# Kernel tuning notes

Measured on AMD Instinct MI355X. Metric: run time of the kernel, lower is better.

Reference implementation:

```python
import jax, jax.numpy as jnp
import numpy as np

N = 4096
BATCH = 256
N_IO = 16
EPS = 1.1920929e-07  # torch RMSNorm default eps = finfo(float32).eps


def setup_inputs() -> dict:
    key = jax.random.key(0)
    k_x, k_w = jax.random.split(key)
    x_input = jax.random.normal(k_x, (BATCH, N), dtype=jnp.float32)
    # orthogonal init for W
    a = jax.random.normal(k_w, (N, N), dtype=jnp.float32)
    q, r = jnp.linalg.qr(a)
    W = q * jnp.sign(jnp.diag(r))[None, :]
    B = jnp.zeros((N,), dtype=jnp.float32)
    input_scale = jnp.ones((N_IO,), dtype=jnp.float32)
    output_scale = jnp.ones((N_IO,), dtype=jnp.float32)
    norm_weight = jnp.ones((N,), dtype=jnp.float32)  # RMSNorm elementwise affine
    input_pos = jnp.arange(N_IO, dtype=jnp.int32)            # ids 0..15
    output_pos = jnp.arange(N_IO, dtype=jnp.int32) + (N - N_IO)  # ids 4080..4095
    return {
        "x_input": x_input, "W": W, "B": B,
        "input_scale": input_scale, "output_scale": output_scale,
        "norm_weight": norm_weight,
        "input_pos": input_pos, "output_pos": output_pos,
        "steps": 16,
    }


def reference(x_input, W, B, input_scale, output_scale, norm_weight,
              input_pos, output_pos, steps):
    # dropout is identity in eval mode (rate 0.0)
    def step(h, inj):
        signal = h @ W + B + inj                      # [batch, N]
        a = jnp.tanh(signal)
        ms = jnp.mean(a * a, axis=-1, keepdims=True)
        return a * jax.lax.rsqrt(ms + EPS) * norm_weight

    # pulse mode: scaled input injected only at t == 0
    inj0 = x_input.at[:, input_pos].multiply(input_scale)
    h0 = jnp.zeros_like(x_input)                      # fresh state
    h1 = step(h0, inj0)

    def body(h, _):
        hn = step(h, 0.0)
        return hn, hn

    h_final, rest = jax.lax.scan(body, h1, None, length=steps - 1)  # rest: [steps-1, batch, N]
    outs = jnp.concatenate([h1[:, None, :], jnp.swapaxes(rest, 0, 1)], axis=1)  # [batch, steps, N]
    outs = outs.at[:, :, output_pos].multiply(output_scale)
    return outs, h_final
```

## Files before the change

kernel.cpp:

```cpp
#include <hip/hip_runtime.h>
#include <hip/hip_bf16.h>

#define BATCH 256
#define NDIM  4096
#define STEPS 16
#define EPS_RMS 1.1920929e-07f

typedef _Float16 f16x8 __attribute__((ext_vector_type(8)));
typedef float  f32x4  __attribute__((ext_vector_type(4)));
typedef unsigned short u16x4 __attribute__((ext_vector_type(4)));
typedef unsigned int   u32x4 __attribute__((ext_vector_type(4)));

#define AS1 __attribute__((address_space(1)))
#define AS3 __attribute__((address_space(3)))
#define GLDS16(gp, lp) __builtin_amdgcn_global_load_lds( \
    (const AS1 void*)(gp), (AS3 void*)(lp), 16, 0, 0)
#define SBAR() do { asm volatile("" ::: "memory"); \
                    __builtin_amdgcn_s_barrier();  \
                    asm volatile("" ::: "memory"); } while (0)

__device__ __forceinline__ unsigned short f2h(float f) {
  _Float16 h = (_Float16)f;
  union { _Float16 h; unsigned short u; } v; v.h = h; return v.u;
}

__device__ __forceinline__ float block_reduce_sum_512(float v) {
  __shared__ float ws[8];
  __shared__ float tot;
  #pragma unroll
  for (int off = 32; off > 0; off >>= 1) v += __shfl_down(v, off, 64);
  int lane = threadIdx.x & 63, w = threadIdx.x >> 6;
  if (lane == 0) ws[w] = v;
  __syncthreads();
  if (threadIdx.x == 0) {
    float t = 0.f;
    #pragma unroll
    for (int i = 0; i < 8; ++i) t += ws[i];
    tot = t;
  }
  __syncthreads();
  return tot;
}

__global__ __launch_bounds__(256) void transpose_w(
    const float* __restrict__ W, unsigned short* __restrict__ Wt) {
  __shared__ float tile[64][65];
  int n0 = blockIdx.x * 64;
  int k0 = blockIdx.y * 64;
  int t = threadIdx.x;
  int r = t >> 4, c4 = (t & 15) * 4;
  #pragma unroll
  for (int p = 0; p < 4; ++p) {
    f32x4 v = *(const f32x4*)(W + (size_t)(k0 + r + 16 * p) * NDIM + n0 + c4);
    tile[r + 16 * p][c4 + 0] = v[0];
    tile[r + 16 * p][c4 + 1] = v[1];
    tile[r + 16 * p][c4 + 2] = v[2];
    tile[r + 16 * p][c4 + 3] = v[3];
  }
  __syncthreads();
  #pragma unroll
  for (int p = 0; p < 4; ++p) {
    int nr = r + 16 * p;
    u16x4 o;
    #pragma unroll
    for (int j = 0; j < 4; ++j) o[j] = f2h(tile[c4 + j][nr]);
    *(u16x4*)(Wt + (size_t)(n0 + nr) * NDIM + k0 + c4) = o;
  }
}

__global__ void init_colmul(const float* __restrict__ iscale,
                            const float* __restrict__ oscale,
                            const int* __restrict__ ipos, const int* __restrict__ opos,
                            float* __restrict__ icm, float* __restrict__ ocm) {
  int c = blockIdx.x * 256 + threadIdx.x;
  if (c >= NDIM) return;
  float iv = 1.f, ov = 1.f;
  #pragma unroll
  for (int i = 0; i < 16; ++i) {
    if (ipos[i] == c) iv *= iscale[i];
    if (opos[i] == c) ov *= oscale[i];
  }
  icm[c] = iv; ocm[c] = ov;
}

__global__ __launch_bounds__(512) void step0_kernel(
    const float* __restrict__ x, const float* __restrict__ bias,
    const float* __restrict__ icm, const float* __restrict__ nw,
    const float* __restrict__ ocm,
    unsigned short* __restrict__ hbuf, float* __restrict__ out) {
  int row = blockIdx.x;
  int tid = threadIdx.x;
  const float* xr = x + (size_t)row * NDIM;
  float a[8];
  float sq = 0.f;
  #pragma unroll
  for (int p = 0; p < 2; ++p) {
    int c = p * 2048 + tid * 4;
    f32x4 xv = *(const f32x4*)(xr + c);
    f32x4 bv = *(const f32x4*)(bias + c);
    f32x4 ic = *(const f32x4*)(icm + c);
    #pragma unroll
    for (int j = 0; j < 4; ++j) {
      float av = tanhf(bv[j] + xv[j] * ic[j]);
      a[p * 4 + j] = av;
      sq += av * av;
    }
  }
  float tot = block_reduce_sum_512(sq);
  float scale = rsqrtf(tot * (1.0f / NDIM) + EPS_RMS);
  unsigned short* hrow = hbuf + (size_t)row * NDIM;
  float* orow = out + (size_t)row * STEPS * NDIM;
  #pragma unroll
  for (int p = 0; p < 2; ++p) {
    int c = p * 2048 + tid * 4;
    f32x4 nv = *(const f32x4*)(nw + c);
    f32x4 oc = *(const f32x4*)(ocm + c);
    u16x4 hs; f32x4 os;
    #pragma unroll
    for (int j = 0; j < 4; ++j) {
      float h = a[p * 4 + j] * scale * nv[j];
      hs[j] = f2h(h);
      os[j] = h * oc[j];
    }
    *(u16x4*)(hrow + c) = hs;
    *(f32x4*)(orow + c) = os;
  }
}

__global__ __launch_bounds__(256, 2) void gemm_kernel(
    const unsigned short* __restrict__ A,
    const unsigned short* __restrict__ Bt,
    float* __restrict__ pbuf) {
  __shared__ __align__(16) unsigned short As[2][64 * 64];
  __shared__ __align__(16) unsigned short Bs[2][128 * 64];
  const int tid = threadIdx.x;
  const int n0 = blockIdx.x * 128;
  const int m0 = blockIdx.y * 64;
  const int ks = blockIdx.z;
  const int kbase = ks * 1024;
  const int wave = tid >> 6, lane = tid & 63;
  const int wm = (wave >> 1) * 32, wn = (wave & 1) * 64;
  const int l15 = lane & 15;
  const int g = lane >> 4;
  const int q = l15 & 7;
  const int rho = lane >> 3;
  const int koff = ((lane & 7) ^ rho) * 8;

  const unsigned short* aP[2];
  const unsigned short* bP[4];
  #pragma unroll
  for (int i = 0; i < 2; ++i)
    aP[i] = A + (size_t)(m0 + wave * 16 + i * 8 + rho) * NDIM + kbase + koff;
  #pragma unroll
  for (int i = 0; i < 4; ++i)
    bP[i] = Bt + (size_t)(n0 + wave * 32 + i * 8 + rho) * NDIM + kbase + koff;

  f32x4 acc[2][4];
  f32x4 zero = {0.f, 0.f, 0.f, 0.f};
  #pragma unroll
  for (int i = 0; i < 2; ++i)
    #pragma unroll
    for (int j = 0; j < 4; ++j) acc[i][j] = zero;

  #pragma unroll
  for (int i = 0; i < 2; ++i)
    GLDS16(aP[i], &As[0][(wave * 16 + i * 8) * 64]);
  #pragma unroll
  for (int i = 0; i < 4; ++i)
    GLDS16(bP[i], &Bs[0][(wave * 32 + i * 8) * 64]);

  for (int it = 0; it < 16; ++it) {
    const int p = it & 1;
    SBAR();
    if (it < 15) {
      const int kb = (it + 1) * 64;
      #pragma unroll
      for (int i = 0; i < 2; ++i)
        GLDS16(aP[i] + kb, &As[1 - p][(wave * 16 + i * 8) * 64]);
      #pragma unroll
      for (int i = 0; i < 4; ++i)
        GLDS16(bP[i] + kb, &Bs[1 - p][(wave * 32 + i * 8) * 64]);
      asm volatile("s_waitcnt vmcnt(6)" ::: "memory");
    } else {
      asm volatile("s_waitcnt vmcnt(0)" ::: "memory");
    }
    SBAR();
    #pragma unroll
    for (int kk = 0; kk < 2; ++kk) {
      f16x8 af[2], bfr[4];
      #pragma unroll
      for (int mf = 0; mf < 2; ++mf) {
        int row = wm + mf * 16 + l15;
        af[mf] = *(const f16x8*)&As[p][row * 64 + (((kk << 2) + g) ^ q) * 8];
      }
      #pragma unroll
      for (int nf = 0; nf < 4; ++nf) {
        int row = wn + nf * 16 + l15;
        bfr[nf] = *(const f16x8*)&Bs[p][row * 64 + (((kk << 2) + g) ^ q) * 8];
      }
      #pragma unroll
      for (int mf = 0; mf < 2; ++mf)
        #pragma unroll
        for (int nf = 0; nf < 4; ++nf)
          acc[mf][nf] = __builtin_amdgcn_mfma_f32_16x16x32_f16(af[mf], bfr[nf], acc[mf][nf], 0, 0, 0);
    }
  }

  float* pout = pbuf + (size_t)ks * BATCH * NDIM;
  const int crow = (lane >> 4) * 4;
  #pragma unroll
  for (int mf = 0; mf < 2; ++mf) {
    #pragma unroll
    for (int nf = 0; nf < 4; ++nf) {
      int col = n0 + wn + nf * 16 + l15;
      #pragma unroll
      for (int r = 0; r < 4; ++r) {
        int row = m0 + wm + mf * 16 + crow + r;
        pout[(size_t)row * NDIM + col] = acc[mf][nf][r];
      }
    }
  }
}

__global__ __launch_bounds__(512) void normalize_kernel(
    const float* __restrict__ pbuf, const float* __restrict__ bias,
    const float* __restrict__ nw, const float* __restrict__ ocm,
    unsigned short* __restrict__ hbuf, float* __restrict__ out,
    float* __restrict__ hfin, int t, int is_last) {
  const size_t SL = (size_t)BATCH * NDIM;
  int row = blockIdx.x;
  int tid = threadIdx.x;
  const float* p0 = pbuf + (size_t)row * NDIM;
  float a[8];
  float sq = 0.f;
  #pragma unroll
  for (int p = 0; p < 2; ++p) {
    int c = p * 2048 + tid * 4;
    f32x4 s = *(const f32x4*)(p0 + c);
    s += *(const f32x4*)(p0 + SL + c);
    s += *(const f32x4*)(p0 + 2 * SL + c);
    s += *(const f32x4*)(p0 + 3 * SL + c);
    f32x4 bv = *(const f32x4*)(bias + c);
    #pragma unroll
    for (int j = 0; j < 4; ++j) {
      float av = tanhf(s[j] + bv[j]);
      a[p * 4 + j] = av;
      sq += av * av;
    }
  }
  float tot = block_reduce_sum_512(sq);
  float scale = rsqrtf(tot * (1.0f / NDIM) + EPS_RMS);
  unsigned short* hrow = hbuf + (size_t)row * NDIM;
  float* orow = out + ((size_t)row * STEPS + t) * NDIM;
  #pragma unroll
  for (int p = 0; p < 2; ++p) {
    int c = p * 2048 + tid * 4;
    f32x4 nv = *(const f32x4*)(nw + c);
    f32x4 oc = *(const f32x4*)(ocm + c);
    u16x4 hs; f32x4 os; f32x4 hv;
    #pragma unroll
    for (int j = 0; j < 4; ++j) {
      float h = a[p * 4 + j] * scale * nv[j];
      hv[j] = h;
      hs[j] = f2h(h);
      os[j] = h * oc[j];
    }
    *(u16x4*)(hrow + c) = hs;
    *(f32x4*)(orow + c) = os;
    if (is_last) *(f32x4*)(hfin + (size_t)row * NDIM + c) = hv;
  }
}

extern "C" void kernel_launch(void* const* d_in, const int* in_sizes, int n_in,
                              void* d_out, int out_size, void* d_ws, size_t ws_size,
                              hipStream_t stream) {
  (void)in_sizes; (void)n_in; (void)out_size; (void)ws_size;
  const float* x      = (const float*)d_in[0];
  const float* W      = (const float*)d_in[1];
  const float* Bb     = (const float*)d_in[2];
  const float* iscale = (const float*)d_in[3];
  const float* oscale = (const float*)d_in[4];
  const float* nw     = (const float*)d_in[5];
  const int* ipos = (const int*)d_in[6];
  const int* opos = (const int*)d_in[7];

  char* ws = (char*)d_ws;
  unsigned short* Wt   = (unsigned short*)(ws);
  unsigned short* hbuf = (unsigned short*)(ws + 33554432);
  float* icm           = (float*)(ws + 35651584);
  float* ocm           = (float*)(ws + 35667968);
  float* pbuf          = (float*)(ws + 35684352);

  float* out  = (float*)d_out;
  float* hfin = out + (size_t)BATCH * STEPS * NDIM;

  hipLaunchKernelGGL(transpose_w, dim3(64, 64), dim3(256), 0, stream, W, Wt);
  hipLaunchKernelGGL(init_colmul, dim3(16), dim3(256), 0, stream,
                     iscale, oscale, ipos, opos, icm, ocm);
  hipLaunchKernelGGL(step0_kernel, dim3(256), dim3(512), 0, stream,
                     x, Bb, icm, nw, ocm, hbuf, out);
  for (int t = 1; t < STEPS; ++t) {
    hipLaunchKernelGGL(gemm_kernel, dim3(32, 4, 4), dim3(256), 0, stream,
                       hbuf, Wt, pbuf);
    hipLaunchKernelGGL(normalize_kernel, dim3(256), dim3(512), 0, stream,
                       pbuf, Bb, nw, ocm, hbuf, out, hfin, t, (t == STEPS - 1) ? 1 : 0);
  }
}
```

Before: 362.4 us.

## Fuse split-K GEMM with RMSNorm epilogue via atomic counters and ping-pong state

The per-step GEMM and normalize kernels are merged into one launch. GEMM blocks publish completion through per-row-block atomic counters, and the first 256 blocks spin-wait on those counters before each normalizes one batch row. The hidden state is double-buffered so the next step's input is never overwritten while it is still being read. The init_colmul kernel is folded into the transpose kernel, which saves launches. The cost is the in-kernel spin-wait, which assumes all 512 blocks are co-resident, and fewer threads per row in the normalize phase.

```diff
diff --git a/kernel.cpp b/kernel.cpp
--- a/kernel.cpp
+++ b/kernel.cpp
@@ -43,11 +43,27 @@
 }
 
 __global__ __launch_bounds__(256) void transpose_w(
-    const float* __restrict__ W, unsigned short* __restrict__ Wt) {
+    const float* __restrict__ W, unsigned short* __restrict__ Wt,
+    const float* __restrict__ iscale, const float* __restrict__ oscale,
+    const int* __restrict__ ipos, const int* __restrict__ opos,
+    float* __restrict__ icm, float* __restrict__ ocm, int* __restrict__ cnt) {
   __shared__ float tile[64][65];
   int n0 = blockIdx.x * 64;
   int k0 = blockIdx.y * 64;
   int t = threadIdx.x;
+  if (blockIdx.y == 0) {
+    if (blockIdx.x == 0 && t < 64) cnt[t] = 0;
+    if (t < 64) {
+      int c = n0 + t;
+      float iv = 1.f, ov = 1.f;
+      #pragma unroll
+      for (int i = 0; i < 16; ++i) {
+        if (ipos[i] == c) iv *= iscale[i];
+        if (opos[i] == c) ov *= oscale[i];
+      }
+      icm[c] = iv; ocm[c] = ov;
+    }
+  }
   int r = t >> 4, c4 = (t & 15) * 4;
   #pragma unroll
   for (int p = 0; p < 4; ++p) {
@@ -66,21 +82,6 @@
     for (int j = 0; j < 4; ++j) o[j] = f2h(tile[c4 + j][nr]);
     *(u16x4*)(Wt + (size_t)(n0 + nr) * NDIM + k0 + c4) = o;
   }
-}
-
-__global__ void init_colmul(const float* __restrict__ iscale,
-                            const float* __restrict__ oscale,
-                            const int* __restrict__ ipos, const int* __restrict__ opos,
-                            float* __restrict__ icm, float* __restrict__ ocm) {
-  int c = blockIdx.x * 256 + threadIdx.x;
-  if (c >= NDIM) return;
-  float iv = 1.f, ov = 1.f;
-  #pragma unroll
-  for (int i = 0; i < 16; ++i) {
-    if (ipos[i] == c) iv *= iscale[i];
-    if (opos[i] == c) ov *= oscale[i];
-  }
-  icm[c] = iv; ocm[c] = ov;
 }
 
 __global__ __launch_bounds__(512) void step0_kernel(
@@ -127,12 +128,19 @@
   }
 }
 
-__global__ __launch_bounds__(256, 2) void gemm_kernel(
+__global__ __launch_bounds__(256, 2) void fused_step(
     const unsigned short* __restrict__ A,
     const unsigned short* __restrict__ Bt,
-    float* __restrict__ pbuf) {
+    float* __restrict__ pbuf,
+    const float* __restrict__ bias, const float* __restrict__ nw,
+    const float* __restrict__ ocm,
+    unsigned short* __restrict__ hnext,
+    float* __restrict__ out, float* __restrict__ hfin,
+    int* __restrict__ cnt, int t, int is_last) {
   __shared__ __align__(16) unsigned short As[2][64 * 64];
   __shared__ __align__(16) unsigned short Bs[2][128 * 64];
+  __shared__ float rws[4];
+  __shared__ float rtot;
   const int tid = threadIdx.x;
   const int n0 = blockIdx.x * 128;
   const int m0 = blockIdx.y * 64;
@@ -206,36 +214,47 @@
     }
   }
 
-  float* pout = pbuf + (size_t)ks * BATCH * NDIM;
-  const int crow = (lane >> 4) * 4;
-  #pragma unroll
-  for (int mf = 0; mf < 2; ++mf) {
-    #pragma unroll
-    for (int nf = 0; nf < 4; ++nf) {
-      int col = n0 + wn + nf * 16 + l15;
-      #pragma unroll
-      for (int r = 0; r < 4; ++r) {
-        int row = m0 + wm + mf * 16 + crow + r;
-        pout[(size_t)row * NDIM + col] = acc[mf][nf][r];
+  {
+    float* pout = pbuf + (size_t)ks * BATCH * NDIM;
+    const int crow = g * 4;
+    #pragma unroll
+    for (int mf = 0; mf < 2; ++mf) {
+      #pragma unroll
+      for (int nf = 0; nf < 4; ++nf) {
+        int col = n0 + wn + nf * 16 + l15;
+        #pragma unroll
+        for (int r = 0; r < 4; ++r) {
+          int row = m0 + wm + mf * 16 + crow + r;
+          pout[(size_t)row * NDIM + col] = acc[mf][nf][r];
+        }
       }
     }
   }
-}
-
-__global__ __launch_bounds__(512) void normalize_kernel(
-    const float* __restrict__ pbuf, const float* __restrict__ bias,
-    const float* __restrict__ nw, const float* __restrict__ ocm,
-    unsigned short* __restrict__ hbuf, float* __restrict__ out,
-    float* __restrict__ hfin, int t, int is_last) {
+
+  __syncthreads();
+  if (tid == 0) {
+    __threadfence();
+    __hip_atomic_fetch_add(&cnt[blockIdx.y], 1, __ATOMIC_RELEASE,
+                           __HIP_MEMORY_SCOPE_AGENT);
+  }
+
+  const int bid = blockIdx.x + 32 * blockIdx.y + 128 * blockIdx.z;
+  if (bid >= BATCH) return;
+  const int row = bid;
+  if (tid == 0) {
+    while (__hip_atomic_load(&cnt[row >> 6], __ATOMIC_ACQUIRE,
+                             __HIP_MEMORY_SCOPE_AGENT) < 128)
+      __builtin_amdgcn_s_sleep(2);
+  }
+  __syncthreads();
+
   const size_t SL = (size_t)BATCH * NDIM;
-  int row = blockIdx.x;
-  int tid = threadIdx.x;
   const float* p0 = pbuf + (size_t)row * NDIM;
-  float a[8];
+  float a[16];
   float sq = 0.f;
   #pragma unroll
-  for (int p = 0; p < 2; ++p) {
-    int c = p * 2048 + tid * 4;
+  for (int p = 0; p < 4; ++p) {
+    int c = p * 1024 + tid * 4;
     f32x4 s = *(const f32x4*)(p0 + c);
     s += *(const f32x4*)(p0 + SL + c);
     s += *(const f32x4*)(p0 + 2 * SL + c);
@@ -248,13 +267,20 @@
       sq += av * av;
     }
   }
-  float tot = block_reduce_sum_512(sq);
-  float scale = rsqrtf(tot * (1.0f / NDIM) + EPS_RMS);
-  unsigned short* hrow = hbuf + (size_t)row * NDIM;
+  {
+    #pragma unroll
+    for (int off = 32; off > 0; off >>= 1) sq += __shfl_down(sq, off, 64);
+    if (lane == 0) rws[wave] = sq;
+    __syncthreads();
+    if (tid == 0) rtot = rws[0] + rws[1] + rws[2] + rws[3];
+    __syncthreads();
+  }
+  float scale = rsqrtf(rtot * (1.0f / NDIM) + EPS_RMS);
+  unsigned short* hrow = hnext + (size_t)row * NDIM;
   float* orow = out + ((size_t)row * STEPS + t) * NDIM;
   #pragma unroll
-  for (int p = 0; p < 2; ++p) {
-    int c = p * 2048 + tid * 4;
+  for (int p = 0; p < 4; ++p) {
+    int c = p * 1024 + tid * 4;
     f32x4 nv = *(const f32x4*)(nw + c);
     f32x4 oc = *(const f32x4*)(ocm + c);
     u16x4 hs; f32x4 os; f32x4 hv;
@@ -286,23 +312,25 @@
 
   char* ws = (char*)d_ws;
   unsigned short* Wt   = (unsigned short*)(ws);
-  unsigned short* hbuf = (unsigned short*)(ws + 33554432);
-  float* icm           = (float*)(ws + 35651584);
-  float* ocm           = (float*)(ws + 35667968);
-  float* pbuf          = (float*)(ws + 35684352);
+  unsigned short* hA   = (unsigned short*)(ws + 33554432);
+  unsigned short* hB   = (unsigned short*)(ws + 35651584);
+  float* icm           = (float*)(ws + 37748736);
+  float* ocm           = (float*)(ws + 37765120);
+  int*   cnt           = (int*)(ws + 37781504);
+  float* pbuf          = (float*)(ws + 37782528);
 
   float* out  = (float*)d_out;
   float* hfin = out + (size_t)BATCH * STEPS * NDIM;
 
-  hipLaunchKernelGGL(transpose_w, dim3(64, 64), dim3(256), 0, stream, W, Wt);
-  hipLaunchKernelGGL(init_colmul, dim3(16), dim3(256), 0, stream,
-                     iscale, oscale, ipos, opos, icm, ocm);
+  hipLaunchKernelGGL(transpose_w, dim3(64, 64), dim3(256), 0, stream,
+                     W, Wt, iscale, oscale, ipos, opos, icm, ocm, cnt);
   hipLaunchKernelGGL(step0_kernel, dim3(256), dim3(512), 0, stream,
-                     x, Bb, icm, nw, ocm, hbuf, out);
+                     x, Bb, icm, nw, ocm, hA, out);
   for (int t = 1; t < STEPS; ++t) {
-    hipLaunchKernelGGL(gemm_kernel, dim3(32, 4, 4), dim3(256), 0, stream,
-                       hbuf, Wt, pbuf);
-    hipLaunchKernelGGL(normalize_kernel, dim3(256), dim3(512), 0, stream,
-                       pbuf, Bb, nw, ocm, hbuf, out, hfin, t, (t == STEPS - 1) ? 1 : 0);
-  }
-}
+    const unsigned short* Ap = ((t - 1) & 1) ? hB : hA;
+    unsigned short* Ac = (t & 1) ? hB : hA;
+    hipLaunchKernelGGL(fused_step, dim3(32, 4, 4), dim3(256), 0, stream,
+                       Ap, Wt, pbuf, Bb, nw, ocm, Ac, out, hfin,
+                       cnt + 4 * t, t, (t == STEPS - 1) ? 1 : 0);
+  }
+}
```

Result: slower. 1.318 ms (+263.7%).
